# Kernel optimization log

Measured on AMD Instinct MI355X. Metric: run time of the kernel, lower is better.

Reference implementation:

```python
import jax, jax.numpy as jnp
import numpy as np

N_NODES = 50000
N_EDGES = 300000
DIM = 256
ALPHA = 0.1  # residual mixing with initial features, as passed in forward


def gcn_layer(x0, x, edge_idx, W):
    """One GraphConvolution call: mean neighbor aggregation over the edge
    list, GCNII-style residual mix with initial features x0, then linear."""
    src, dst = edge_idx[0], edge_idx[1]
    msgs = x[src]  # [E, D] gather
    agg = jax.ops.segment_sum(msgs, dst, num_segments=x.shape[0])
    deg = jax.ops.segment_sum(jnp.ones((src.shape[0],), x.dtype), dst,
                              num_segments=x.shape[0])
    agg = agg / jnp.maximum(deg, 1.0)[:, None]
    h = ALPHA * x0 + (1.0 - ALPHA) * agg
    return h @ W


def setup_inputs() -> dict:
    key = jax.random.key(0)
    k1, k2, k3 = jax.random.split(key, 3)
    x = jax.random.normal(k1, (N_NODES, DIM), dtype=jnp.float32)
    edge_idx = jax.random.randint(k2, (2, N_EDGES), 0, N_NODES, dtype=jnp.int64)
    W = jax.random.normal(k3, (DIM, DIM), dtype=jnp.float32) / np.sqrt(DIM)
    return {"drug_cell_pair_feature": x, "edge_idx": edge_idx, "W": W}


def reference(drug_cell_pair_feature, edge_idx, W):
    x0 = drug_cell_pair_feature
    out = jax.nn.relu(gcn_layer(x0, x0, edge_idx, W))
    for _ in range(4):  # 4 more identical calls, always mixing with x0
        out = jax.nn.relu(gcn_layer(x0, out, edge_idx, W))
    return out
```

## Files before the change

kernel.cpp:

```cpp
#include <hip/hip_runtime.h>

#define DIM 256
#define SCAN_B 256

typedef __attribute__((ext_vector_type(8))) short short8;
typedef __attribute__((ext_vector_type(4))) float f32x4;

__device__ __forceinline__ unsigned short f32_to_bf16(float x) {
    unsigned int u = __float_as_uint(x);
    unsigned int r = u + 0x7FFFu + ((u >> 16) & 1u);
    return (unsigned short)(r >> 16);
}
__device__ __forceinline__ float bf16_to_f32(unsigned short h) {
    return __uint_as_float(((unsigned int)h) << 16);
}

__device__ __forceinline__ void load_lds16(const void* g, void* l) {
    __builtin_amdgcn_global_load_lds(
        (const __attribute__((address_space(1))) unsigned int*)g,
        (__attribute__((address_space(3))) unsigned int*)l, 16, 0, 0);
}

__global__ void deg_kernel(const int* __restrict__ dst, int E, int* __restrict__ deg) {
    int e = blockIdx.x * blockDim.x + threadIdx.x;
    if (e < E) atomicAdd(&deg[dst[e]], 1);
}

__global__ void scan1_kernel(const int* __restrict__ deg, int N,
                             int* __restrict__ excl, int* __restrict__ bsums) {
    __shared__ int s[SCAN_B];
    int tid = threadIdx.x;
    int i = blockIdx.x * SCAN_B + tid;
    int v = (i < N) ? deg[i] : 0;
    s[tid] = v;
    __syncthreads();
    #pragma unroll
    for (int off = 1; off < SCAN_B; off <<= 1) {
        int t = (tid >= off) ? s[tid - off] : 0;
        __syncthreads();
        s[tid] += t;
        __syncthreads();
    }
    if (i <= N) excl[i] = s[tid] - v;
    if (tid == SCAN_B - 1) bsums[blockIdx.x] = s[tid];
}

__global__ void scan2_kernel(int* __restrict__ bsums, int nb) {
    __shared__ int s[SCAN_B];
    int tid = threadIdx.x;
    int v = (tid < nb) ? bsums[tid] : 0;
    s[tid] = v;
    __syncthreads();
    #pragma unroll
    for (int off = 1; off < SCAN_B; off <<= 1) {
        int t = (tid >= off) ? s[tid - off] : 0;
        __syncthreads();
        s[tid] += t;
        __syncthreads();
    }
    if (tid < nb) bsums[tid] = s[tid] - v;
}

__global__ void scan3_kernel(const int* __restrict__ excl, const int* __restrict__ bsums,
                             const int* __restrict__ deg, int N,
                             int* __restrict__ row_start, float* __restrict__ inv_deg) {
    int i = blockIdx.x * SCAN_B + threadIdx.x;
    if (i <= N) row_start[i] = excl[i] + bsums[blockIdx.x];
    if (i < N) inv_deg[i] = 1.0f / (float)max(deg[i], 1);
}

__global__ void fill_kernel(const int* __restrict__ src, const int* __restrict__ dst, int E,
                            const int* __restrict__ row_start, int* __restrict__ cursor,
                            int* __restrict__ csr_src) {
    int e = blockIdx.x * blockDim.x + threadIdx.x;
    if (e < E) {
        int d = dst[e];
        int pos = row_start[d] + atomicAdd(&cursor[d], 1);
        csr_src[pos] = src[e];
    }
}

__global__ void wprep_kernel(const float* __restrict__ W, unsigned short* __restrict__ Wt) {
    int k = blockIdx.x;
    int n = threadIdx.x;
    Wt[n * DIM + k] = f32_to_bf16(W[k * DIM + n]);
}

__global__ void xprep_kernel(const float* __restrict__ x, unsigned short* __restrict__ act,
                             unsigned short* __restrict__ x0b, int n4) {
    int i = blockIdx.x * blockDim.x + threadIdx.x;
    if (i < n4) {
        float4 v = ((const float4*)x)[i];
        ushort4 o;
        o.x = f32_to_bf16(v.x); o.y = f32_to_bf16(v.y);
        o.z = f32_to_bf16(v.z); o.w = f32_to_bf16(v.w);
        ((ushort4*)act)[i] = o;
        ((ushort4*)x0b)[i] = o;
    }
}

__global__ __launch_bounds__(256) void aggregate_kernel(
    const unsigned short* __restrict__ xh, const unsigned short* __restrict__ x0b,
    const int* __restrict__ row_start, const int* __restrict__ csr_src,
    const float* __restrict__ inv_deg,
    unsigned short* __restrict__ h, int N)
{
    int node = blockIdx.x * 4 + (threadIdx.x >> 6);
    if (node >= N) return;
    int c = (threadIdx.x & 63) * 4;

    int beg = row_start[node];
    int end = row_start[node + 1];

    float a0 = 0.f, a1 = 0.f, a2 = 0.f, a3 = 0.f;
    int e = beg;
    for (; e + 4 <= end; e += 4) {
        int s0 = csr_src[e];
        int s1 = csr_src[e + 1];
        int s2 = csr_src[e + 2];
        int s3 = csr_src[e + 3];
        ushort4 v0 = *(const ushort4*)(xh + (size_t)s0 * DIM + c);
        ushort4 v1 = *(const ushort4*)(xh + (size_t)s1 * DIM + c);
        ushort4 v2 = *(const ushort4*)(xh + (size_t)s2 * DIM + c);
        ushort4 v3 = *(const ushort4*)(xh + (size_t)s3 * DIM + c);
        a0 += (bf16_to_f32(v0.x) + bf16_to_f32(v1.x)) + (bf16_to_f32(v2.x) + bf16_to_f32(v3.x));
        a1 += (bf16_to_f32(v0.y) + bf16_to_f32(v1.y)) + (bf16_to_f32(v2.y) + bf16_to_f32(v3.y));
        a2 += (bf16_to_f32(v0.z) + bf16_to_f32(v1.z)) + (bf16_to_f32(v2.z) + bf16_to_f32(v3.z));
        a3 += (bf16_to_f32(v0.w) + bf16_to_f32(v1.w)) + (bf16_to_f32(v2.w) + bf16_to_f32(v3.w));
    }
    for (; e < end; e++) {
        int s0 = csr_src[e];
        ushort4 v0 = *(const ushort4*)(xh + (size_t)s0 * DIM + c);
        a0 += bf16_to_f32(v0.x);
        a1 += bf16_to_f32(v0.y);
        a2 += bf16_to_f32(v0.z);
        a3 += bf16_to_f32(v0.w);
    }

    float scale = 0.9f * inv_deg[node];
    ushort4 xv = *(const ushort4*)(x0b + (size_t)node * DIM + c);
    ushort4 o;
    o.x = f32_to_bf16(0.1f * bf16_to_f32(xv.x) + scale * a0);
    o.y = f32_to_bf16(0.1f * bf16_to_f32(xv.y) + scale * a1);
    o.z = f32_to_bf16(0.1f * bf16_to_f32(xv.z) + scale * a2);
    o.w = f32_to_bf16(0.1f * bf16_to_f32(xv.w) + scale * a3);
    *(ushort4*)(h + (size_t)node * DIM + c) = o;
}

template <bool LAST>
__global__ __launch_bounds__(256) void gemm_kernel(
    const unsigned short* __restrict__ h, const unsigned short* __restrict__ Wt,
    float* __restrict__ out_f32, unsigned short* __restrict__ out_bf16, int N)
{
    __shared__ unsigned short As[128 * 32];
    __shared__ unsigned short Bs[128 * 32];

    const int t    = threadIdx.x;
    const int w    = t >> 6;
    const int lane = t & 63;
    const int lm   = lane & 15;
    const int q    = lane >> 4;
    const int wm   = w >> 1, wn = w & 1;
    const int m0   = blockIdx.x * 128;
    const int n0   = blockIdx.y * 128;

    const int sr = t >> 2;
    const int sg = (t & 3) * 8;

    f32x4 acc[4][4];
    #pragma unroll
    for (int mi = 0; mi < 4; mi++)
        #pragma unroll
        for (int ni = 0; ni < 4; ni++)
            acc[mi][ni] = (f32x4){0.f, 0.f, 0.f, 0.f};

    for (int kb = 0; kb < DIM; kb += 32) {
        __syncthreads();
        #pragma unroll
        for (int half = 0; half < 2; half++) {
            int r = half * 64 + sr;
            int ldso = (half * 256 + t) * 8;
            load_lds16(h  + (size_t)(m0 + r) * DIM + kb + sg, &As[ldso]);
            load_lds16(Wt + (size_t)(n0 + r) * DIM + kb + sg, &Bs[ldso]);
        }
        __syncthreads();

        short8 a[4];
        #pragma unroll
        for (int mi = 0; mi < 4; mi++) {
            int row = wm * 64 + mi * 16 + lm;
            a[mi] = *(const short8*)&As[row * 32 + q * 8];
        }
        #pragma unroll
        for (int ni = 0; ni < 4; ni++) {
            int row = wn * 64 + ni * 16 + lm;
            short8 b = *(const short8*)&Bs[row * 32 + q * 8];
            #pragma unroll
            for (int mi = 0; mi < 4; mi++)
                acc[mi][ni] = __builtin_amdgcn_mfma_f32_16x16x32_bf16(a[mi], b, acc[mi][ni], 0, 0, 0);
        }
    }

    #pragma unroll
    for (int mi = 0; mi < 4; mi++) {
        const int rowb = m0 + wm * 64 + mi * 16 + q * 4;
        #pragma unroll
        for (int ni = 0; ni < 4; ni++) {
            const int col = n0 + wn * 64 + ni * 16 + lm;
            #pragma unroll
            for (int r = 0; r < 4; r++) {
                int row = rowb + r;
                if (row < N) {
                    float v = fmaxf(acc[mi][ni][r], 0.0f);
                    if (LAST) out_f32[(size_t)row * DIM + col] = v;
                    else      out_bf16[(size_t)row * DIM + col] = f32_to_bf16(v);
                }
            }
        }
    }
}

extern "C" void kernel_launch(void* const* d_in, const int* in_sizes, int n_in,
                              void* d_out, int out_size, void* d_ws, size_t ws_size,
                              hipStream_t stream) {
    const float* x0  = (const float*)d_in[0];
    const int*   ei  = (const int*)d_in[1];
    const float* W   = (const float*)d_in[2];
    float*       out = (float*)d_out;

    const int N = in_sizes[0] / DIM;
    const int E = in_sizes[1] / 2;
    const int N_pad = (N + 127) & ~127;
    const int* src = ei;
    const int* dst = ei + E;

    const int nb = (N + 1 + SCAN_B - 1) / SCAN_B;

    char* ws = (char*)d_ws;
    size_t off = 0;
    auto alloc = [&](size_t bytes) { char* p = ws + off; off += (bytes + 15) & ~size_t(15); return p; };
    unsigned short* h       = (unsigned short*)alloc((size_t)N_pad * DIM * 2);
    unsigned short* act     = (unsigned short*)alloc((size_t)N_pad * DIM * 2);
    unsigned short* x0b     = (unsigned short*)alloc((size_t)N_pad * DIM * 2);
    unsigned short* Wt      = (unsigned short*)alloc((size_t)DIM * DIM * 2);
    float* inv_deg  = (float*)alloc((size_t)N * 4);
    int*   deg      = (int*)  alloc((size_t)N * 4);
    int*   row_start= (int*)  alloc((size_t)(N + 1) * 4);
    int*   excl     = (int*)  alloc((size_t)(N + 1) * 4);
    int*   cursor   = (int*)  alloc((size_t)N * 4);
    int*   bsums    = (int*)  alloc((size_t)nb * 4);
    int*   csr_src  = (int*)  alloc((size_t)E * 4);

    hipMemsetAsync(deg, 0, (size_t)N * 4, stream);
    hipMemsetAsync(cursor, 0, (size_t)N * 4, stream);
    deg_kernel<<<(E + 255) / 256, 256, 0, stream>>>(dst, E, deg);
    scan1_kernel<<<nb, SCAN_B, 0, stream>>>(deg, N, excl, bsums);
    scan2_kernel<<<1, SCAN_B, 0, stream>>>(bsums, nb);
    scan3_kernel<<<nb, SCAN_B, 0, stream>>>(excl, bsums, deg, N, row_start, inv_deg);
    fill_kernel<<<(E + 255) / 256, 256, 0, stream>>>(src, dst, E, row_start, cursor, csr_src);
    wprep_kernel<<<DIM, DIM, 0, stream>>>(W, Wt);
    const int n4 = N * DIM / 4;
    xprep_kernel<<<(n4 + 255) / 256, 256, 0, stream>>>(x0, act, x0b, n4);

    dim3 ggrid(N_pad / 128, 2);
    for (int layer = 0; layer < 5; layer++) {
        aggregate_kernel<<<(N + 3) / 4, 256, 0, stream>>>(act, x0b, row_start, csr_src,
                                                          inv_deg, h, N);
        if (layer == 4)
            gemm_kernel<true><<<ggrid, 256, 0, stream>>>(h, Wt, out, nullptr, N);
        else
            gemm_kernel<false><<<ggrid, 256, 0, stream>>>(h, Wt, nullptr, act, N);
    }
}
```

Measured before the change: 396.0 us.

## Vectorize aggregation to 16-byte gathers with half-wave edge split, merge prep kernels

The aggregation kernel now has each half-wave handle alternate edges, with every lane loading 8 bf16 values (16 bytes). The two halves are combined with a cross-lane shuffle, so each gather instruction covers more bytes and there are fewer load instructions per edge. The weight and feature prep kernels are merged into one launch, the redundant act copy of x0 is dropped (layer 0 gathers from x0b), and the two memsets become one. The shuffle reduction and the idle upper half-wave during writeback add a little overhead, and odd-degree tails leave half the wave idle.

```diff
diff --git a/kernel.cpp b/kernel.cpp
--- a/kernel.cpp
+++ b/kernel.cpp
@@ -4,6 +4,7 @@
 #define SCAN_B 256
 
 typedef __attribute__((ext_vector_type(8))) short short8;
+typedef __attribute__((ext_vector_type(8))) unsigned short u16x8;
 typedef __attribute__((ext_vector_type(4))) float f32x4;
 
 __device__ __forceinline__ unsigned short f32_to_bf16(float x) {
@@ -80,22 +81,22 @@
     }
 }
 
-__global__ void wprep_kernel(const float* __restrict__ W, unsigned short* __restrict__ Wt) {
-    int k = blockIdx.x;
-    int n = threadIdx.x;
-    Wt[n * DIM + k] = f32_to_bf16(W[k * DIM + n]);
-}
-
-__global__ void xprep_kernel(const float* __restrict__ x, unsigned short* __restrict__ act,
-                             unsigned short* __restrict__ x0b, int n4) {
-    int i = blockIdx.x * blockDim.x + threadIdx.x;
-    if (i < n4) {
-        float4 v = ((const float4*)x)[i];
-        ushort4 o;
-        o.x = f32_to_bf16(v.x); o.y = f32_to_bf16(v.y);
-        o.z = f32_to_bf16(v.z); o.w = f32_to_bf16(v.w);
-        ((ushort4*)act)[i] = o;
-        ((ushort4*)x0b)[i] = o;
+__global__ void prep_kernel(const float* __restrict__ W, unsigned short* __restrict__ Wt,
+                            const float* __restrict__ x0, unsigned short* __restrict__ x0b,
+                            int n4) {
+    int b = blockIdx.x;
+    if (b < DIM) {
+        int k = b, n = threadIdx.x;
+        Wt[n * DIM + k] = f32_to_bf16(W[k * DIM + n]);
+    } else {
+        int i = (b - DIM) * 256 + threadIdx.x;
+        if (i < n4) {
+            float4 v = ((const float4*)x0)[i];
+            ushort4 o;
+            o.x = f32_to_bf16(v.x); o.y = f32_to_bf16(v.y);
+            o.z = f32_to_bf16(v.z); o.w = f32_to_bf16(v.w);
+            ((ushort4*)x0b)[i] = o;
+        }
     }
 }
 
@@ -107,44 +108,52 @@
 {
     int node = blockIdx.x * 4 + (threadIdx.x >> 6);
     if (node >= N) return;
-    int c = (threadIdx.x & 63) * 4;
+    const int lane = threadIdx.x & 63;
+    const int half = lane >> 5;
+    const int c    = (lane & 31) * 8;
 
     int beg = row_start[node];
     int end = row_start[node + 1];
 
-    float a0 = 0.f, a1 = 0.f, a2 = 0.f, a3 = 0.f;
+    float a[8];
+    #pragma unroll
+    for (int j = 0; j < 8; j++) a[j] = 0.f;
+
     int e = beg;
     for (; e + 4 <= end; e += 4) {
+        int s0 = csr_src[e + half];
+        int s1 = csr_src[e + 2 + half];
+        u16x8 v0 = *(const u16x8*)(xh + (size_t)s0 * DIM + c);
+        u16x8 v1 = *(const u16x8*)(xh + (size_t)s1 * DIM + c);
+        #pragma unroll
+        for (int j = 0; j < 8; j++) a[j] += bf16_to_f32(v0[j]) + bf16_to_f32(v1[j]);
+    }
+    if (e + 2 <= end) {
+        int s0 = csr_src[e + half];
+        u16x8 v0 = *(const u16x8*)(xh + (size_t)s0 * DIM + c);
+        #pragma unroll
+        for (int j = 0; j < 8; j++) a[j] += bf16_to_f32(v0[j]);
+        e += 2;
+    }
+    if (e < end && half == 0) {
         int s0 = csr_src[e];
-        int s1 = csr_src[e + 1];
-        int s2 = csr_src[e + 2];
-        int s3 = csr_src[e + 3];
-        ushort4 v0 = *(const ushort4*)(xh + (size_t)s0 * DIM + c);
-        ushort4 v1 = *(const ushort4*)(xh + (size_t)s1 * DIM + c);
-        ushort4 v2 = *(const ushort4*)(xh + (size_t)s2 * DIM + c);
-        ushort4 v3 = *(const ushort4*)(xh + (size_t)s3 * DIM + c);
-        a0 += (bf16_to_f32(v0.x) + bf16_to_f32(v1.x)) + (bf16_to_f32(v2.x) + bf16_to_f32(v3.x));
-        a1 += (bf16_to_f32(v0.y) + bf16_to_f32(v1.y)) + (bf16_to_f32(v2.y) + bf16_to_f32(v3.y));
-        a2 += (bf16_to_f32(v0.z) + bf16_to_f32(v1.z)) + (bf16_to_f32(v2.z) + bf16_to_f32(v3.z));
-        a3 += (bf16_to_f32(v0.w) + bf16_to_f32(v1.w)) + (bf16_to_f32(v2.w) + bf16_to_f32(v3.w));
-    }
-    for (; e < end; e++) {
-        int s0 = csr_src[e];
-        ushort4 v0 = *(const ushort4*)(xh + (size_t)s0 * DIM + c);
-        a0 += bf16_to_f32(v0.x);
-        a1 += bf16_to_f32(v0.y);
-        a2 += bf16_to_f32(v0.z);
-        a3 += bf16_to_f32(v0.w);
-    }
-
-    float scale = 0.9f * inv_deg[node];
-    ushort4 xv = *(const ushort4*)(x0b + (size_t)node * DIM + c);
-    ushort4 o;
-    o.x = f32_to_bf16(0.1f * bf16_to_f32(xv.x) + scale * a0);
-    o.y = f32_to_bf16(0.1f * bf16_to_f32(xv.y) + scale * a1);
-    o.z = f32_to_bf16(0.1f * bf16_to_f32(xv.z) + scale * a2);
-    o.w = f32_to_bf16(0.1f * bf16_to_f32(xv.w) + scale * a3);
-    *(ushort4*)(h + (size_t)node * DIM + c) = o;
+        u16x8 v0 = *(const u16x8*)(xh + (size_t)s0 * DIM + c);
+        #pragma unroll
+        for (int j = 0; j < 8; j++) a[j] += bf16_to_f32(v0[j]);
+    }
+
+    #pragma unroll
+    for (int j = 0; j < 8; j++) a[j] += __shfl_xor(a[j], 32);
+
+    if (half == 0) {
+        float scale = 0.9f * inv_deg[node];
+        u16x8 xv = *(const u16x8*)(x0b + (size_t)node * DIM + c);
+        u16x8 o;
+        #pragma unroll
+        for (int j = 0; j < 8; j++)
+            o[j] = f32_to_bf16(0.1f * bf16_to_f32(xv[j]) + scale * a[j]);
+        *(u16x8*)(h + (size_t)node * DIM + c) = o;
+    }
 }
 
 template <bool LAST>
@@ -244,27 +253,26 @@
     unsigned short* x0b     = (unsigned short*)alloc((size_t)N_pad * DIM * 2);
     unsigned short* Wt      = (unsigned short*)alloc((size_t)DIM * DIM * 2);
     float* inv_deg  = (float*)alloc((size_t)N * 4);
-    int*   deg      = (int*)  alloc((size_t)N * 4);
+    int*   deg      = (int*)  alloc((size_t)N * 4 * 2);
+    int*   cursor   = deg + N;
     int*   row_start= (int*)  alloc((size_t)(N + 1) * 4);
     int*   excl     = (int*)  alloc((size_t)(N + 1) * 4);
-    int*   cursor   = (int*)  alloc((size_t)N * 4);
     int*   bsums    = (int*)  alloc((size_t)nb * 4);
     int*   csr_src  = (int*)  alloc((size_t)E * 4);
 
-    hipMemsetAsync(deg, 0, (size_t)N * 4, stream);
-    hipMemsetAsync(cursor, 0, (size_t)N * 4, stream);
+    hipMemsetAsync(deg, 0, (size_t)N * 4 * 2, stream);
     deg_kernel<<<(E + 255) / 256, 256, 0, stream>>>(dst, E, deg);
     scan1_kernel<<<nb, SCAN_B, 0, stream>>>(deg, N, excl, bsums);
     scan2_kernel<<<1, SCAN_B, 0, stream>>>(bsums, nb);
     scan3_kernel<<<nb, SCAN_B, 0, stream>>>(excl, bsums, deg, N, row_start, inv_deg);
     fill_kernel<<<(E + 255) / 256, 256, 0, stream>>>(src, dst, E, row_start, cursor, csr_src);
-    wprep_kernel<<<DIM, DIM, 0, stream>>>(W, Wt);
     const int n4 = N * DIM / 4;
-    xprep_kernel<<<(n4 + 255) / 256, 256, 0, stream>>>(x0, act, x0b, n4);
+    prep_kernel<<<DIM + (n4 + 255) / 256, 256, 0, stream>>>(W, Wt, x0, x0b, n4);
 
     dim3 ggrid(N_pad / 128, 2);
     for (int layer = 0; layer < 5; layer++) {
-        aggregate_kernel<<<(N + 3) / 4, 256, 0, stream>>>(act, x0b, row_start, csr_src,
+        const unsigned short* gsrc = (layer == 0) ? x0b : act;
+        aggregate_kernel<<<(N + 3) / 4, 256, 0, stream>>>(gsrc, x0b, row_start, csr_src,
                                                           inv_deg, h, N);
         if (layer == 4)
             gemm_kernel<true><<<ggrid, 256, 0, stream>>>(h, Wt, out, nullptr, N);
```

New measurement: 384.3 us. -2.9%, faster.
